# Optimization experiments

Measured on AMD Instinct MI355X. Metric: run time of the kernel, lower is better.

## Reference

```python
import jax, jax.numpy as jnp
import numpy as np

HIDDEN = 8   # TrajGRU hidden channels (hardcoded in module)
L = 5        # number of flow links
NEG = 0.2    # leaky relu slope (HKO-7 RNN_ACT_TYPE)


def conv2d(x, w, b, pad):
    y = jax.lax.conv_general_dilated(x, w, (1, 1), [(pad, pad), (pad, pad)],
                                     dimension_numbers=('NCHW', 'OIHW', 'NCHW'))
    return y + b[None, :, None, None]


def leaky(x):
    return jnp.where(x >= 0, x, NEG * x)


def bilinear_sample(im, x, y):
    # im: (C,H,W); x,y: (H,W) pixel coords; zero padding outside (grid_sample align_corners=True)
    C, H, W = im.shape
    x0 = jnp.floor(x); y0 = jnp.floor(y)
    wx = x - x0; wy = y - y0

    def g(ix, iy):
        valid = (ix >= 0) & (ix <= W - 1) & (iy >= 0) & (iy <= H - 1)
        ic = jnp.clip(ix, 0, W - 1).astype(jnp.int32)
        jc = jnp.clip(iy, 0, H - 1).astype(jnp.int32)
        return jnp.where(valid[None], im[:, jc, ic], 0.0)

    v00 = g(x0, y0); v01 = g(x0 + 1, y0)
    v10 = g(x0, y0 + 1); v11 = g(x0 + 1, y0 + 1)
    top = v00 * (1 - wx) + v01 * wx
    bot = v10 * (1 - wx) + v11 * wx
    return top * (1 - wy) + bot * wy


def trajgru_step(x, h, w_i2h, b_i2h, w_i2f, b_i2f, w_h2f, b_h2f,
                 w_flows, b_flows, w_ret, b_ret):
    B, C, H, W = h.shape
    # flow generator
    f = leaky(conv2d(x, w_i2f, b_i2f, 2) + conv2d(h, w_h2f, b_h2f, 2))
    flows = conv2d(f, w_flows, b_flows, 2).reshape(B, L, 2, H, W)
    # warp hidden along each link: wrap(h, -flow) => sample at grid - flow
    xx = jnp.arange(W, dtype=jnp.float32)[None, :] * jnp.ones((H, 1), jnp.float32)
    yy = jnp.arange(H, dtype=jnp.float32)[:, None] * jnp.ones((1, W), jnp.float32)
    cx = xx - flows[:, :, 0]  # (B,L,H,W)
    cy = yy - flows[:, :, 1]
    warp_b = jax.vmap(lambda hb, cxb, cyb:
                      jax.vmap(lambda a, b2: bilinear_sample(hb, a, b2))(cxb, cyb))
    warped = warp_b(h, cx, cy).reshape(B, L * C, H, W)  # (B, L*C, H, W)
    h2h = conv2d(warped, w_ret, b_ret, 0)
    i2h = conv2d(x, w_i2h, b_i2h, 1)
    i_r, i_u, i_m = jnp.split(i2h, 3, axis=1)
    h_r, h_u, h_m = jnp.split(h2h, 3, axis=1)
    reset = jax.nn.sigmoid(i_r + h_r)
    update = jax.nn.sigmoid(i_u + h_u)
    new_mem = leaky(i_m + reset * h_m)
    return update * h + (1.0 - update) * new_mem


def setup_inputs():
    key = jax.random.key(0)
    ks = jax.random.split(key, 16)
    B, T_in, T_out, H, W = 32, 12, 12, 128, 128
    in_ch = T_in + T_out
    p = lambda k, shape: 0.1 * jax.random.normal(k, shape, dtype=jnp.float32)
    return {
        'radar_data': jax.random.normal(ks[0], (B, T_in, 1, H, W), dtype=jnp.float32),
        'first_stage_pred': jax.random.normal(ks[1], (B, T_out, 1, H, W), dtype=jnp.float32),
        'w_conv_in': p(ks[2], (HIDDEN, in_ch, 3, 3)), 'b_conv_in': p(ks[3], (HIDDEN,)),
        'w_i2h': p(ks[4], (3 * HIDDEN, HIDDEN, 3, 3)), 'b_i2h': p(ks[5], (3 * HIDDEN,)),
        'w_i2f': p(ks[6], (32, HIDDEN, 5, 5)), 'b_i2f': p(ks[7], (32,)),
        'w_h2f': p(ks[8], (32, HIDDEN, 5, 5)), 'b_h2f': p(ks[9], (32,)),
        'w_flows': p(ks[10], (2 * L, 32, 5, 5)), 'b_flows': p(ks[11], (2 * L,)),
        'w_ret': p(ks[12], (3 * HIDDEN, L * HIDDEN, 1, 1)), 'b_ret': p(ks[13], (3 * HIDDEN,)),
        'w_conv_out': p(ks[14], (T_out, HIDDEN, 1, 1)), 'b_conv_out': p(ks[15], (T_out,)),
    }


def reference(radar_data, first_stage_pred, w_conv_in, b_conv_in, w_i2h, b_i2h,
              w_i2f, b_i2f, w_h2f, b_h2f, w_flows, b_flows, w_ret, b_ret,
              w_conv_out, b_conv_out):
    B, T_in, _, H, W = radar_data.shape
    T_out = first_stage_pred.shape[1]
    x = jnp.concatenate([radar_data.reshape(B, T_in, H, W),
                         first_stage_pred.reshape(B, T_out, H, W)], axis=1)
    x = conv2d(x, w_conv_in, b_conv_in, 1)          # (B, hidden, H, W)
    h0 = jnp.zeros((B, HIDDEN, H, W), x.dtype)       # TrajGRU zero initial state
    h = trajgru_step(x, h0, w_i2h, b_i2h, w_i2f, b_i2f, w_h2f, b_h2f,
                     w_flows, b_flows, w_ret, b_ret)  # seq_len == 1
    out = conv2d(h, w_conv_out, b_conv_out, 0)       # (B, pred_len, H, W)
    return out.reshape(B, T_out, 1, H, W)
```

## Files before the change

kernel.cpp:

```cpp
#include <hip/hip_runtime.h>
#include <hip/hip_bf16.h>


typedef __fp16   h2f __attribute__((ext_vector_type(2)));
typedef _Float16 v4h __attribute__((ext_vector_type(4)));
typedef _Float16 v8h __attribute__((ext_vector_type(8)));
typedef float    v4f __attribute__((ext_vector_type(4)));

#define HW 128
#define SPITCH 24
#define PCOLS 36
#define NPOS  720
#define NSLOT 1440
#define SXW   34
#define SXN   612

#define WB_HOFF 4608
#define FLT_OFF 16384
#define N_PREP  7828

__global__ __launch_bounds__(256)
void prep(const float* __restrict__ w_in,  const float* __restrict__ b_in,
          const float* __restrict__ w_i2h, const float* __restrict__ b_i2h,
          const float* __restrict__ b_ret, const float* __restrict__ w_out,
          const float* __restrict__ b_out, void* __restrict__ ws)
{
    int idx = blockIdx.x * 256 + threadIdx.x;
    _Float16* wh = (_Float16*)ws;
    float* fw = (float*)((char*)ws + FLT_OFF);
    if (idx < 4608) {
        int j = idx & 7, r = idx >> 3;
        int lane = r & 63, sg = r >> 6;
        int g = sg % 3, s = sg / 3;
        int quad = lane >> 4, n = lane & 15;
        int tap = s * 4 + quad;
        float v = (n < 8 && tap < 9) ? w_in[n*216 + (g*8 + j)*9 + tap] : 0.f;
        wh[idx] = (_Float16)v;
    } else if (idx < 7680) {
        int i2 = idx - 4608;
        int j = i2 & 7, r = i2 >> 3;
        int lane = r & 63; r >>= 6;
        int nt = r & 1, s = r >> 1;
        int quad = lane >> 4, n = lane & 15;
        int kk = s * 32 + quad * 8 + j;
        int t = kk >> 3, m = kk & 7;
        int o = nt * 16 + n;
        float v = (t < 9 && o < 24) ? w_i2h[o*72 + m*9 + t] : 0.f;
        wh[WB_HOFF + i2] = (_Float16)v;
    } else if (idx < N_PREP) {
        int j = idx - 7680;
        float v;
        if (j < 32) {
            int c = j & 7, sel = j >> 3;
            v = (sel==0) ? b_i2h[c]    + b_ret[c]
              : (sel==1) ? b_i2h[8+c]  + b_ret[8+c]
              : (sel==2) ? b_i2h[16+c] : b_ret[16+c];
        } else if (j < 128) v = w_out[j-32];
        else if (j < 140)   v = b_out[j-128];
        else                v = b_in[j-140];
        fw[j] = v;
    }
}

__device__ __forceinline__ void pack12(_Float16* dst, const float* v)
{
    union { h2f h2[4]; v8h h8; } u;
    union { h2f h2[2]; v4h h4; } w;
#pragma unroll
    for (int k = 0; k < 4; ++k)
        u.h2[k] = __builtin_amdgcn_cvt_pkrtz(v[2*k], v[2*k+1]);
    w.h2[0] = __builtin_amdgcn_cvt_pkrtz(v[8], v[9]);
    w.h2[1] = __builtin_amdgcn_cvt_pkrtz(v[10], v[11]);
    *(v8h*)&dst[0] = u.h8;
    *(v4h*)&dst[8] = w.h4;
}

__global__ __launch_bounds__(512, 8)
void radar2_mfma(const float* __restrict__ radar,
                 const float* __restrict__ pred,
                 const void*  __restrict__ ws,
                 float* __restrict__ out)
{
    __shared__ __align__(16) char pool[NPOS * SPITCH * 2];
    _Float16* s_in = (_Float16*)pool;
    _Float16* s_x  = (_Float16*)pool;
    float*    s_hc = (float*)(pool + 9792);

    const _Float16* wh = (const _Float16*)ws;
    const float* fw = (const float*)((const char*)ws + FLT_OFF);

    const int tid  = threadIdx.x;
    const int lane = tid & 63;
    const int wave = tid >> 6;
    const int quad = lane >> 4;
    const int col  = lane & 15;

    const int id   = blockIdx.x;
    const int b    = (id & 7) * 4 + (id >> 8);
    const int tile = (id >> 3) & 31;
    const int ty0  = (tile >> 2) << 4;
    const int tx0  = (tile & 3) << 5;

    const float* rb = radar + (((size_t)b * 12) << 14);
    const float* pb = pred  + (((size_t)b * 12) << 14);

    const int s0 = tid, s1 = tid + 512, s2 = tid + 1024;
    const int p0 = s0 >> 1, p1 = s1 >> 1, p2 = s2 >> 1;
    const bool has2 = (s2 < NSLOT);

    const int ly0 = p0 / PCOLS, lx0 = p0 - PCOLS * ly0;
    const int gy0 = ty0 + ly0 - 2, gx0 = tx0 + lx0 - 2;
    const bool in0 = ((unsigned)gy0 < HW) & ((unsigned)gx0 < HW);
    const int off0 = (gy0 << 7) + gx0;
    const float* src0 = (s0 & 1) ? pb : rb;

    const int ly1 = p1 / PCOLS, lx1 = p1 - PCOLS * ly1;
    const int gy1 = ty0 + ly1 - 2, gx1 = tx0 + lx1 - 2;
    const bool in1 = ((unsigned)gy1 < HW) & ((unsigned)gx1 < HW);
    const int off1 = (gy1 << 7) + gx1;
    const float* src1 = (s1 & 1) ? pb : rb;

    const int ly2 = p2 / PCOLS, lx2 = p2 - PCOLS * ly2;
    const int gy2 = ty0 + ly2 - 2, gx2 = tx0 + lx2 - 2;
    const bool in2 = has2 & ((unsigned)gy2 < HW) & ((unsigned)gx2 < HW);
    const int off2 = (gy2 << 7) + gx2;
    const float* src2 = (s2 & 1) ? pb : rb;

    float v0[12], v1[12], v2[12];
#pragma unroll
    for (int c = 0; c < 12; ++c) v0[c] = in0 ? src0[((size_t)c << 14) + off0] : 0.f;
#pragma unroll
    for (int c = 0; c < 12; ++c) v1[c] = in1 ? src1[((size_t)c << 14) + off1] : 0.f;
#pragma unroll
    for (int c = 0; c < 12; ++c) v2[c] = in2 ? src2[((size_t)c << 14) + off2] : 0.f;

    pack12(&s_in[p0 * SPITCH + (s0 & 1) * 12], v0);
    pack12(&s_in[p1 * SPITCH + (s1 & 1) * 12], v1);
    if (has2) pack12(&s_in[p2 * SPITCH + (s2 & 1) * 12], v2);
    __syncthreads();

    int toffA[3];
#pragma unroll
    for (int s = 0; s < 3; ++s) {
        int t = s * 4 + quad;
        toffA[s] = (t < 9) ? ((t / 3) * PCOLS + (t % 3)) * SPITCH : 0;
    }
    int pbase[5];
#pragma unroll
    for (int t = 0; t < 5; ++t) {
        int p = (wave + 8 * t) * 16 + col; if (p > SXN - 1) p = SXN - 1;
        pbase[t] = ((p / SXW) * PCOLS + (p % SXW)) * SPITCH;
    }
    v4f accA[5];
#pragma unroll
    for (int t = 0; t < 5; ++t) accA[t] = (v4f){0.f, 0.f, 0.f, 0.f};
#pragma unroll
    for (int s = 0; s < 3; ++s) {
        v8h bg[3];
#pragma unroll
        for (int g = 0; g < 3; ++g)
            bg[g] = *(const v8h*)&wh[((s * 3 + g) * 64 + lane) * 8];
#pragma unroll
        for (int t = 0; t < 5; ++t) {
            if (wave + 8 * t < 39) {
                int ab = pbase[t] + toffA[s];
#pragma unroll
                for (int g = 0; g < 3; ++g) {
                    v8h a = *(const v8h*)&s_in[ab + g * 8];
                    accA[t] = __builtin_amdgcn_mfma_f32_16x16x32_f16(a, bg[g], accA[t], 0, 0, 0);
                }
            }
        }
    }
    __syncthreads();

    const float binv = fw[140 + (col & 7)];
    if (col < 8) {
#pragma unroll
        for (int t = 0; t < 5; ++t) {
            int mt = wave + 8 * t;
            if (mt < 39) {
#pragma unroll
                for (int r = 0; r < 4; ++r) {
                    int pa = mt * 16 + quad * 4 + r;
                    int py = pa / SXW, px = pa - SXW * py;
                    bool ok = ((unsigned)(ty0 + py - 1) < HW) &&
                              ((unsigned)(tx0 + px - 1) < HW);
                    if (pa < SXN)
                        s_x[pa * 8 + col] = (_Float16)(ok ? accA[t][r] + binv : 0.f);
                }
            }
        }
    }
    __syncthreads();

    int toff2[3];
#pragma unroll
    for (int s = 0; s < 3; ++s) {
        int t = s * 4 + quad;
        toff2[s] = (t < 9) ? ((t / 3) * SXW + (t % 3)) * 8 : 0;
    }
    int abase2[4];
#pragma unroll
    for (int t = 0; t < 4; ++t) {
        int q = (wave + 8 * t) * 16 + col;
        abase2[t] = ((q >> 5) * SXW + (q & 31)) * 8;
    }
    v4f acc0[4], acc1[4];
#pragma unroll
    for (int t = 0; t < 4; ++t) {
        acc0[t] = (v4f){0.f, 0.f, 0.f, 0.f};
        acc1[t] = (v4f){0.f, 0.f, 0.f, 0.f};
    }
#pragma unroll
    for (int s = 0; s < 3; ++s) {
        v8h b0 = *(const v8h*)&wh[WB_HOFF + ((s * 2 + 0) * 64 + lane) * 8];
        v8h b1 = *(const v8h*)&wh[WB_HOFF + ((s * 2 + 1) * 64 + lane) * 8];
#pragma unroll
        for (int t = 0; t < 4; ++t) {
            v8h a = *(const v8h*)&s_x[abase2[t] + toff2[s]];
            acc0[t] = __builtin_amdgcn_mfma_f32_16x16x32_f16(a, b0, acc0[t], 0, 0, 0);
            acc1[t] = __builtin_amdgcn_mfma_f32_16x16x32_f16(a, b1, acc1[t], 0, 0, 0);
        }
    }

    const int c7 = lane & 7;
    const float g0v = fw[c7], g1v = fw[8 + c7], g2v = fw[16 + c7], g3v = fw[24 + c7];
#pragma unroll
    for (int t = 0; t < 4; ++t) {
        int mt = wave + 8 * t;
#pragma unroll
        for (int r = 0; r < 4; ++r) {
            float iu = __shfl_xor(acc0[t][r], 8, 64);
            if (col < 8) {
                float rr = 1.f / (1.f + __expf(-(acc0[t][r] + g0v)));
                float uu = 1.f / (1.f + __expf(-(iu + g1v)));
                float mm = acc1[t][r] + g2v + rr * g3v;
                mm = (mm >= 0.f) ? mm : 0.2f * mm;
                s_hc[(mt * 16 + quad * 4 + r) * 9 + c7] = (1.f - uu) * mm;
            }
        }
    }
    __syncthreads();

    float h[8];
#pragma unroll
    for (int c = 0; c < 8; ++c) h[c] = s_hc[tid * 9 + c];
    const float* wout = fw + 32;
    const float* bout = fw + 128;
    const int oy = tid >> 5, ox = tid & 31;
    float* op = out + (((size_t)b * 12) << 14) + ((ty0 + oy) << 7) + (tx0 + ox);
#pragma unroll
    for (int t = 0; t < 12; ++t) {
        float o = bout[t];
#pragma unroll
        for (int c = 0; c < 8; ++c) o = fmaf(h[c], wout[t * 8 + c], o);
        op[(size_t)t << 14] = o;
    }
}

extern "C" void kernel_launch(void* const* d_in, const int* in_sizes, int n_in,
                              void* d_out, int out_size, void* d_ws, size_t ws_size,
                              hipStream_t stream) {
    (void)in_sizes; (void)n_in; (void)ws_size; (void)out_size;
    const float* radar = (const float*)d_in[0];
    const float* pred  = (const float*)d_in[1];
    const float* w_in  = (const float*)d_in[2];
    const float* b_in  = (const float*)d_in[3];
    const float* w_i2h = (const float*)d_in[4];
    const float* b_i2h = (const float*)d_in[5];
    const float* b_ret = (const float*)d_in[13];
    const float* w_out = (const float*)d_in[14];
    const float* b_out = (const float*)d_in[15];

    prep<<<(N_PREP + 255) / 256, 256, 0, stream>>>(w_in, b_in, w_i2h, b_i2h,
                                                   b_ret, w_out, b_out, d_ws);

    radar2_mfma<<<dim3(1024), dim3(512), 0, stream>>>(radar, pred, d_ws, (float*)d_out);
}
```

Measured before the change: 147.0 us.

## Split fused conv kernel into conv_in and gate kernels via fp16 global buffer

Splits the single fused kernel into two. The first computes the input conv over 8x32 tiles with a 1-pixel halo and writes the fp16 x tensor to workspace. The second reads it directly from global memory with bounds masks to compute the i2h conv and gating. This removes the redundant halo recomputation of conv_in and the 2-pixel input halo loads, and shrinks blocks to 256 threads. In exchange it adds an extra launch and a global round-trip of the x tensor, with uncoalesced 16-byte neighbor reads.

```diff
diff --git a/kernel.cpp b/kernel.cpp
--- a/kernel.cpp
+++ b/kernel.cpp
@@ -9,14 +9,13 @@
 
 #define HW 128
 #define SPITCH 24
-#define PCOLS 36
-#define NPOS  720
-#define NSLOT 1440
-#define SXW   34
-#define SXN   612
+#define PC1   34
+#define NP1   340
+#define NSLOT1 680
 
 #define WB_HOFF 4608
 #define FLT_OFF 16384
+#define X_OFF   65536
 #define N_PREP  7828
 
 __global__ __launch_bounds__(256)
@@ -75,16 +74,19 @@
     *(v4h*)&dst[8] = w.h4;
 }
 
-__global__ __launch_bounds__(512, 8)
-void radar2_mfma(const float* __restrict__ radar,
-                 const float* __restrict__ pred,
-                 const void*  __restrict__ ws,
-                 float* __restrict__ out)
-{
-    __shared__ __align__(16) char pool[NPOS * SPITCH * 2];
-    _Float16* s_in = (_Float16*)pool;
-    _Float16* s_x  = (_Float16*)pool;
-    float*    s_hc = (float*)(pool + 9792);
+__device__ __forceinline__ void tile_decode(int id, int& b, int& ty0, int& tx0)
+{
+    b   = (id & 7) * 4 + (id >> 9);
+    int tile = (id >> 3) & 63;
+    ty0 = (tile >> 2) << 3;
+    tx0 = (tile & 3) << 5;
+}
+
+__global__ __launch_bounds__(256, 8)
+void k1_convin(const float* __restrict__ radar, const float* __restrict__ pred,
+               const void* __restrict__ ws, _Float16* __restrict__ xw)
+{
+    __shared__ __align__(16) _Float16 s_in[NP1 * SPITCH];
 
     const _Float16* wh = (const _Float16*)ws;
     const float* fw = (const float*)((const char*)ws + FLT_OFF);
@@ -95,33 +97,30 @@
     const int quad = lane >> 4;
     const int col  = lane & 15;
 
-    const int id   = blockIdx.x;
-    const int b    = (id & 7) * 4 + (id >> 8);
-    const int tile = (id >> 3) & 31;
-    const int ty0  = (tile >> 2) << 4;
-    const int tx0  = (tile & 3) << 5;
+    int b, ty0, tx0;
+    tile_decode(blockIdx.x, b, ty0, tx0);
 
     const float* rb = radar + (((size_t)b * 12) << 14);
     const float* pb = pred  + (((size_t)b * 12) << 14);
 
-    const int s0 = tid, s1 = tid + 512, s2 = tid + 1024;
+    const int s0 = tid, s1 = tid + 256, s2 = tid + 512;
     const int p0 = s0 >> 1, p1 = s1 >> 1, p2 = s2 >> 1;
-    const bool has2 = (s2 < NSLOT);
-
-    const int ly0 = p0 / PCOLS, lx0 = p0 - PCOLS * ly0;
-    const int gy0 = ty0 + ly0 - 2, gx0 = tx0 + lx0 - 2;
+    const bool has2 = (s2 < NSLOT1);
+
+    const int ly0 = p0 / PC1, lx0 = p0 - PC1 * ly0;
+    const int gy0 = ty0 + ly0 - 1, gx0 = tx0 + lx0 - 1;
     const bool in0 = ((unsigned)gy0 < HW) & ((unsigned)gx0 < HW);
     const int off0 = (gy0 << 7) + gx0;
     const float* src0 = (s0 & 1) ? pb : rb;
 
-    const int ly1 = p1 / PCOLS, lx1 = p1 - PCOLS * ly1;
-    const int gy1 = ty0 + ly1 - 2, gx1 = tx0 + lx1 - 2;
+    const int ly1 = p1 / PC1, lx1 = p1 - PC1 * ly1;
+    const int gy1 = ty0 + ly1 - 1, gx1 = tx0 + lx1 - 1;
     const bool in1 = ((unsigned)gy1 < HW) & ((unsigned)gx1 < HW);
     const int off1 = (gy1 << 7) + gx1;
     const float* src1 = (s1 & 1) ? pb : rb;
 
-    const int ly2 = p2 / PCOLS, lx2 = p2 - PCOLS * ly2;
-    const int gy2 = ty0 + ly2 - 2, gx2 = tx0 + lx2 - 2;
+    const int ly2 = p2 / PC1, lx2 = p2 - PC1 * ly2;
+    const int gy2 = ty0 + ly2 - 1, gx2 = tx0 + lx2 - 1;
     const bool in2 = has2 & ((unsigned)gy2 < HW) & ((unsigned)gx2 < HW);
     const int off2 = (gy2 << 7) + gx2;
     const float* src2 = (s2 & 1) ? pb : rb;
@@ -143,17 +142,17 @@
 #pragma unroll
     for (int s = 0; s < 3; ++s) {
         int t = s * 4 + quad;
-        toffA[s] = (t < 9) ? ((t / 3) * PCOLS + (t % 3)) * SPITCH : 0;
-    }
-    int pbase[5];
-#pragma unroll
-    for (int t = 0; t < 5; ++t) {
-        int p = (wave + 8 * t) * 16 + col; if (p > SXN - 1) p = SXN - 1;
-        pbase[t] = ((p / SXW) * PCOLS + (p % SXW)) * SPITCH;
-    }
-    v4f accA[5];
-#pragma unroll
-    for (int t = 0; t < 5; ++t) accA[t] = (v4f){0.f, 0.f, 0.f, 0.f};
+        toffA[s] = (t < 9) ? ((t / 3) * PC1 + (t % 3)) * SPITCH : 0;
+    }
+    int pbase[4];
+#pragma unroll
+    for (int t = 0; t < 4; ++t) {
+        int p = (wave + 4 * t) * 16 + col;
+        pbase[t] = ((p >> 5) * PC1 + (p & 31)) * SPITCH;
+    }
+    v4f accA[4];
+#pragma unroll
+    for (int t = 0; t < 4; ++t) accA[t] = (v4f){0.f, 0.f, 0.f, 0.f};
 #pragma unroll
     for (int s = 0; s < 3; ++s) {
         v8h bg[3];
@@ -161,51 +160,65 @@
         for (int g = 0; g < 3; ++g)
             bg[g] = *(const v8h*)&wh[((s * 3 + g) * 64 + lane) * 8];
 #pragma unroll
-        for (int t = 0; t < 5; ++t) {
-            if (wave + 8 * t < 39) {
-                int ab = pbase[t] + toffA[s];
-#pragma unroll
-                for (int g = 0; g < 3; ++g) {
-                    v8h a = *(const v8h*)&s_in[ab + g * 8];
-                    accA[t] = __builtin_amdgcn_mfma_f32_16x16x32_f16(a, bg[g], accA[t], 0, 0, 0);
-                }
+        for (int t = 0; t < 4; ++t) {
+            int ab = pbase[t] + toffA[s];
+#pragma unroll
+            for (int g = 0; g < 3; ++g) {
+                v8h a = *(const v8h*)&s_in[ab + g * 8];
+                accA[t] = __builtin_amdgcn_mfma_f32_16x16x32_f16(a, bg[g], accA[t], 0, 0, 0);
             }
         }
     }
-    __syncthreads();
 
     const float binv = fw[140 + (col & 7)];
     if (col < 8) {
 #pragma unroll
-        for (int t = 0; t < 5; ++t) {
-            int mt = wave + 8 * t;
-            if (mt < 39) {
-#pragma unroll
-                for (int r = 0; r < 4; ++r) {
-                    int pa = mt * 16 + quad * 4 + r;
-                    int py = pa / SXW, px = pa - SXW * py;
-                    bool ok = ((unsigned)(ty0 + py - 1) < HW) &&
-                              ((unsigned)(tx0 + px - 1) < HW);
-                    if (pa < SXN)
-                        s_x[pa * 8 + col] = (_Float16)(ok ? accA[t][r] + binv : 0.f);
-                }
+        for (int t = 0; t < 4; ++t) {
+#pragma unroll
+            for (int r = 0; r < 4; ++r) {
+                int p = (wave + 4 * t) * 16 + quad * 4 + r;
+                int gy = ty0 + (p >> 5), gx = tx0 + (p & 31);
+                h2f one = __builtin_amdgcn_cvt_pkrtz(accA[t][r] + binv, 0.f);
+                xw[((((size_t)b << 14) + (gy << 7) + gx) << 3) + col] = one[0];
             }
         }
     }
-    __syncthreads();
-
-    int toff2[3];
+}
+
+__global__ __launch_bounds__(256, 8)
+void k2_rest(const _Float16* __restrict__ xw, const void* __restrict__ ws,
+             float* __restrict__ out)
+{
+    __shared__ float s_hc[256 * 9];
+
+    const _Float16* wh = (const _Float16*)ws;
+    const float* fw = (const float*)((const char*)ws + FLT_OFF);
+
+    const int tid  = threadIdx.x;
+    const int lane = tid & 63;
+    const int wave = tid >> 6;
+    const int quad = lane >> 4;
+    const int col  = lane & 15;
+
+    int b, ty0, tx0;
+    tile_decode(blockIdx.x, b, ty0, tx0);
+
+    int dys[3], dxs[3];
 #pragma unroll
     for (int s = 0; s < 3; ++s) {
         int t = s * 4 + quad;
-        toff2[s] = (t < 9) ? ((t / 3) * SXW + (t % 3)) * 8 : 0;
-    }
-    int abase2[4];
-#pragma unroll
-    for (int t = 0; t < 4; ++t) {
-        int q = (wave + 8 * t) * 16 + col;
-        abase2[t] = ((q >> 5) * SXW + (q & 31)) * 8;
-    }
+        dys[s] = (t < 9) ? (t / 3) - 1 : 0;
+        dxs[s] = (t < 9) ? (t % 3) - 1 : 0;
+    }
+    int gyv[4], gxv[4];
+#pragma unroll
+    for (int t = 0; t < 4; ++t) {
+        int p = (wave + 4 * t) * 16 + col;
+        gyv[t] = ty0 + (p >> 5);
+        gxv[t] = tx0 + (p & 31);
+    }
+    const _Float16* xb = xw + (((size_t)b << 14) << 3);
+
     v4f acc0[4], acc1[4];
 #pragma unroll
     for (int t = 0; t < 4; ++t) {
@@ -218,7 +231,11 @@
         v8h b1 = *(const v8h*)&wh[WB_HOFF + ((s * 2 + 1) * 64 + lane) * 8];
 #pragma unroll
         for (int t = 0; t < 4; ++t) {
-            v8h a = *(const v8h*)&s_x[abase2[t] + toff2[s]];
+            int sy = gyv[t] + dys[s], sx = gxv[t] + dxs[s];
+            bool ok = ((unsigned)sy < HW) & ((unsigned)sx < HW);
+            int idx = ok ? ((sy << 7) + sx) : 0;
+            v8h a = *(const v8h*)&xb[(size_t)idx << 3];
+            if (!ok) a = (v8h)(_Float16)0.f;
             acc0[t] = __builtin_amdgcn_mfma_f32_16x16x32_f16(a, b0, acc0[t], 0, 0, 0);
             acc1[t] = __builtin_amdgcn_mfma_f32_16x16x32_f16(a, b1, acc1[t], 0, 0, 0);
         }
@@ -228,7 +245,7 @@
     const float g0v = fw[c7], g1v = fw[8 + c7], g2v = fw[16 + c7], g3v = fw[24 + c7];
 #pragma unroll
     for (int t = 0; t < 4; ++t) {
-        int mt = wave + 8 * t;
+        int mt = wave + 4 * t;
 #pragma unroll
         for (int r = 0; r < 4; ++r) {
             float iu = __shfl_xor(acc0[t][r], 8, 64);
@@ -273,8 +290,10 @@
     const float* w_out = (const float*)d_in[14];
     const float* b_out = (const float*)d_in[15];
 
+    _Float16* xw = (_Float16*)((char*)d_ws + X_OFF);
+
     prep<<<(N_PREP + 255) / 256, 256, 0, stream>>>(w_in, b_in, w_i2h, b_i2h,
                                                    b_ret, w_out, b_out, d_ws);
-
-    radar2_mfma<<<dim3(1024), dim3(512), 0, stream>>>(radar, pred, d_ws, (float*)d_out);
-}
+    k1_convin<<<dim3(2048), dim3(256), 0, stream>>>(radar, pred, d_ws, xw);
+    k2_rest<<<dim3(2048), dim3(256), 0, stream>>>(xw, d_ws, (float*)d_out);
+}
```

Measured after the change: 152.2 us. 3.5% more time.
